# Kernel tuning notes

Hardware: AMD Instinct MI355X
Metric: run time of the kernel (lower is better)

## Reference

```python
import jax, jax.numpy as jnp
import numpy as np

B, E, D, H = 4096, 16, 512, 2048

def setup_inputs() -> dict:
    key = jax.random.key(0)
    k1, k2, k3, k4 = jax.random.split(key, 4)
    semantic_vec = jax.random.normal(k1, (B, D), dtype=jnp.float32)
    field_centers = jax.random.normal(k2, (E, D), dtype=jnp.float32)
    # Kaiming-uniform-ish Linear init scale
    lim = 1.0 / np.sqrt(D)
    W = jax.random.uniform(k3, (E, H, D), dtype=jnp.float32, minval=-lim, maxval=lim)
    b = jax.random.uniform(k4, (E, H), dtype=jnp.float32, minval=-lim, maxval=lim)
    return {"semantic_vec": semantic_vec, "field_centers": field_centers, "W": W, "b": b}

def reference(semantic_vec, field_centers, W, b):
    # Each expert e: relu((x - c_e) @ W_e^T + b_e); sum over experts.
    # Use linearity: (x - c_e) @ W_e^T = x @ W_e^T - c_e @ W_e^T, avoiding the [B,E,D] offsets tensor.
    xw = jnp.einsum('bd,ehd->beh', semantic_vec, W)          # [B,E,H]
    cw = jnp.einsum('ed,ehd->eh', field_centers, W)          # [E,H]
    pre = xw - cw[None, :, :] + b[None, :, :]                # [B,E,H]
    feature_anchor = jnp.sum(jax.nn.relu(pre), axis=1)       # [B,H]
    return feature_anchor
```

## Files before the change

kernel.cpp:

```cpp
#include <hip/hip_runtime.h>
#include <hip/hip_bf16.h>
#include <stdint.h>
#include <stddef.h>


#define B_DIM 4096
#define E_DIM 16
#define D_DIM 512
#define H_DIM 2048

typedef short bf16x8 __attribute__((ext_vector_type(8)));
typedef float f32x4 __attribute__((ext_vector_type(4)));

__device__ __forceinline__ short f2bf(float f) {
  __hip_bfloat16 h = __float2bfloat16(f);
  return *reinterpret_cast<short*>(&h);
}

__device__ __forceinline__ bf16x8 cvt8(float4 a, float4 b) {
  bf16x8 v;
  v[0] = f2bf(a.x); v[1] = f2bf(a.y); v[2] = f2bf(a.z); v[3] = f2bf(a.w);
  v[4] = f2bf(b.x); v[5] = f2bf(b.y); v[6] = f2bf(b.z); v[7] = f2bf(b.w);
  return v;
}

__device__ __forceinline__ void async_copy16(const void* gptr, void* lptr) {
  __builtin_amdgcn_global_load_lds(
      (const __attribute__((address_space(1))) void*)gptr,
      (__attribute__((address_space(3))) void*)lptr,
      16, 0, 0);
}

__global__ __launch_bounds__(256) void prep_w(
    const float* __restrict__ W, const float* __restrict__ C,
    const float* __restrict__ bias, __hip_bfloat16* __restrict__ Wb,
    float* __restrict__ bias2) {
  const int gw = (blockIdx.x * 256 + threadIdx.x) >> 6;
  const int lane = threadIdx.x & 63;
  const int e = gw >> 11;

  const float* wr = W + (size_t)gw * D_DIM + lane * 8;
  const float* cr = C + (size_t)e * D_DIM + lane * 8;
  float4 w0 = *(const float4*)(wr);
  float4 w1 = *(const float4*)(wr + 4);
  float4 c0 = *(const float4*)(cr);
  float4 c1 = *(const float4*)(cr + 4);

  *(bf16x8*)((__hip_bfloat16*)Wb + (size_t)gw * D_DIM + lane * 8) = cvt8(w0, w1);

  float dot = w0.x * c0.x + w0.y * c0.y + w0.z * c0.z + w0.w * c0.w +
              w1.x * c1.x + w1.y * c1.y + w1.z * c1.z + w1.w * c1.w;
#pragma unroll
  for (int off = 32; off > 0; off >>= 1) dot += __shfl_down(dot, off, 64);
  if (lane == 0) bias2[gw] = bias[gw] - dot;
}

__global__ __launch_bounds__(256) void conv_x(
    const float* __restrict__ X, __hip_bfloat16* __restrict__ Xb) {
  const size_t i = ((size_t)blockIdx.x * 256 + threadIdx.x) * 8;
  float4 a = *(const float4*)(X + i);
  float4 b = *(const float4*)(X + i + 4);
  *(bf16x8*)(Xb + i) = cvt8(a, b);
}

__global__ __launch_bounds__(256, 2) void moe_gemm(
    const __hip_bfloat16* __restrict__ Xb,
    const __hip_bfloat16* __restrict__ Wb,
    const float* __restrict__ bias2,
    float* __restrict__ out) {
  __shared__ __align__(16) __hip_bfloat16 As[128 * 32];
  __shared__ __align__(16) __hip_bfloat16 Bs0[128 * 32];
  __shared__ __align__(16) __hip_bfloat16 Bs1[128 * 32];
  __shared__ __align__(16) float biasS[E_DIM * 128];

  const int tid = threadIdx.x;
  const int lane = tid & 63;
  const int wave = tid >> 6;
  const int hi = blockIdx.x & 15;
  const int mi = blockIdx.x >> 4;
  const int m0 = mi * 128;
  const int h0 = hi * 128;

  for (int idx = tid; idx < E_DIM * 128; idx += 256) {
    biasS[idx] = bias2[((idx >> 7) << 11) + h0 + (idx & 127)];
  }

  const int wm = (wave & 1) * 64;
  const int wn = (wave >> 1) * 64;
  const int lm = lane & 15;
  const int q = lane >> 4;

  const int r = tid >> 2;
  const int ql = tid & 3;
  const int fr = (r ^ (r >> 2)) & 3;
  const int srcCol = ((ql ^ fr) << 3);

  const __hip_bfloat16* Asrc0 = Xb + (size_t)(m0 + r) * D_DIM + srcCol;
  const __hip_bfloat16* Asrc1 = Xb + (size_t)(m0 + r + 64) * D_DIM + srcCol;
  const size_t brow0 = (size_t)(h0 + r) * D_DIM + srcCol;
  const size_t brow1 = (size_t)(h0 + r + 64) * D_DIM + srcCol;

  int offA[4], offB[4];
#pragma unroll
  for (int i = 0; i < 4; ++i) {
    const int R = wm + i * 16 + lm;
    const int f = (R ^ (R >> 2)) & 3;
    offA[i] = R * 32 + ((q ^ f) << 3);
  }
#pragma unroll
  for (int j = 0; j < 4; ++j) {
    const int R = wn + j * 16 + lm;
    const int f = (R ^ (R >> 2)) & 3;
    offB[j] = R * 32 + ((q ^ f) << 3);
  }

  f32x4 sum[4][4];
#pragma unroll
  for (int i = 0; i < 4; ++i)
#pragma unroll
    for (int j = 0; j < 4; ++j) sum[i][j] = (f32x4){0.f, 0.f, 0.f, 0.f};

  for (int ep = 0; ep < E_DIM / 2; ++ep) {
    const __hip_bfloat16* B0 = Wb + ((size_t)(2 * ep) << 20);
    const __hip_bfloat16* B1 = Wb + ((size_t)(2 * ep + 1) << 20);

    f32x4 acc0[4][4], acc1[4][4];
#pragma unroll
    for (int i = 0; i < 4; ++i)
#pragma unroll
      for (int j = 0; j < 4; ++j) {
        acc0[i][j] = (f32x4){0.f, 0.f, 0.f, 0.f};
        acc1[i][j] = (f32x4){0.f, 0.f, 0.f, 0.f};
      }

    for (int k = 0; k < D_DIM; k += 32) {
      __syncthreads();
      async_copy16(Asrc0 + k, &As[(size_t)tid * 8]);
      async_copy16(Asrc1 + k, &As[(size_t)(tid + 256) * 8]);
      async_copy16(B0 + brow0 + k, &Bs0[(size_t)tid * 8]);
      async_copy16(B0 + brow1 + k, &Bs0[(size_t)(tid + 256) * 8]);
      async_copy16(B1 + brow0 + k, &Bs1[(size_t)tid * 8]);
      async_copy16(B1 + brow1 + k, &Bs1[(size_t)(tid + 256) * 8]);
      __syncthreads();

      bf16x8 af[4];
#pragma unroll
      for (int i = 0; i < 4; ++i) af[i] = *(const bf16x8*)&As[offA[i]];
#pragma unroll
      for (int j = 0; j < 4; ++j) {
        const bf16x8 b0 = *(const bf16x8*)&Bs0[offB[j]];
#pragma unroll
        for (int i = 0; i < 4; ++i)
          acc0[i][j] = __builtin_amdgcn_mfma_f32_16x16x32_bf16(
              af[i], b0, acc0[i][j], 0, 0, 0);
        const bf16x8 b1 = *(const bf16x8*)&Bs1[offB[j]];
#pragma unroll
        for (int i = 0; i < 4; ++i)
          acc1[i][j] = __builtin_amdgcn_mfma_f32_16x16x32_bf16(
              af[i], b1, acc1[i][j], 0, 0, 0);
      }
    }

#pragma unroll
    for (int j = 0; j < 4; ++j) {
      const float bv0 = biasS[(2 * ep) * 128 + wn + j * 16 + lm];
      const float bv1 = biasS[(2 * ep + 1) * 128 + wn + j * 16 + lm];
#pragma unroll
      for (int i = 0; i < 4; ++i)
#pragma unroll
        for (int t = 0; t < 4; ++t)
          sum[i][j][t] += fmaxf(acc0[i][j][t] + bv0, 0.f) +
                          fmaxf(acc1[i][j][t] + bv1, 0.f);
    }
  }

  const int rbase = q * 4;
#pragma unroll
  for (int i = 0; i < 4; ++i)
#pragma unroll
    for (int j = 0; j < 4; ++j)
#pragma unroll
      for (int t = 0; t < 4; ++t)
        out[(size_t)(m0 + wm + i * 16 + rbase + t) * H_DIM + h0 + wn + j * 16 + lm] =
            sum[i][j][t];
}

__global__ __launch_bounds__(256) void naive_kernel(
    const float* __restrict__ x, const float* __restrict__ c,
    const float* __restrict__ W, const float* __restrict__ bias,
    float* __restrict__ out) {
  const int idx = blockIdx.x * 256 + threadIdx.x;
  const int b = idx >> 11;
  const int h = idx & (H_DIM - 1);
  const float* xr = x + (size_t)b * D_DIM;
  float s = 0.f;
  for (int e = 0; e < E_DIM; ++e) {
    const float* wr = W + ((size_t)e * H_DIM + h) * D_DIM;
    const float* cr = c + (size_t)e * D_DIM;
    float acc = bias[e * H_DIM + h];
    for (int d = 0; d < D_DIM; ++d) acc += (xr[d] - cr[d]) * wr[d];
    s += fmaxf(acc, 0.f);
  }
  out[idx] = s;
}

extern "C" void kernel_launch(void* const* d_in, const int* in_sizes, int n_in,
                              void* d_out, int out_size, void* d_ws, size_t ws_size,
                              hipStream_t stream) {
  const float* x = (const float*)d_in[0];
  const float* c = (const float*)d_in[1];
  const float* W = (const float*)d_in[2];
  const float* b = (const float*)d_in[3];
  float* out = (float*)d_out;

  const size_t sz_wb = (size_t)E_DIM * H_DIM * D_DIM * 2;
  const size_t sz_xb = (size_t)B_DIM * D_DIM * 2;
  const size_t sz_b2 = (size_t)E_DIM * H_DIM * 4;
  const size_t need = sz_wb + sz_xb + sz_b2;

  if (ws_size >= need) {
    __hip_bfloat16* Wb = (__hip_bfloat16*)((char*)d_ws);
    __hip_bfloat16* Xb = (__hip_bfloat16*)((char*)d_ws + sz_wb);
    float* bias2 = (float*)((char*)d_ws + sz_wb + sz_xb);
    prep_w<<<8192, 256, 0, stream>>>(W, c, b, Wb, bias2);
    conv_x<<<1024, 256, 0, stream>>>(x, Xb);
    moe_gemm<<<512, 256, 0, stream>>>(Xb, Wb, bias2, out);
  } else {
    naive_kernel<<<(B_DIM * H_DIM) / 256, 256, 0, stream>>>(x, c, W, b, out);
  }
}
```

Before: 262.0 us.

## Double-buffer LDS tiles and flatten expert/k loops into one pipelined loop

Shared-memory tiles for X and the two expert weight slices are double-buffered so the async global-to-LDS copy for the next k-step is issued before computing on the current one, with a single barrier per step. The expert-pair and k loops are merged into one 128-iteration loop, with the bias+ReLU reduction applied every 16 steps. The XOR swizzle on LDS layout is removed, simplifying addressing but possibly introducing bank conflicts, and LDS usage roughly doubles, which may constrain occupancy.

```diff
diff --git a/kernel.cpp b/kernel.cpp
--- a/kernel.cpp
+++ b/kernel.cpp
@@ -68,9 +68,9 @@
     const __hip_bfloat16* __restrict__ Wb,
     const float* __restrict__ bias2,
     float* __restrict__ out) {
-  __shared__ __align__(16) __hip_bfloat16 As[128 * 32];
-  __shared__ __align__(16) __hip_bfloat16 Bs0[128 * 32];
-  __shared__ __align__(16) __hip_bfloat16 Bs1[128 * 32];
+  __shared__ __align__(16) __hip_bfloat16 As[2][128 * 32];
+  __shared__ __align__(16) __hip_bfloat16 Bs0[2][128 * 32];
+  __shared__ __align__(16) __hip_bfloat16 Bs1[2][128 * 32];
   __shared__ __align__(16) float biasS[E_DIM * 128];
 
   const int tid = threadIdx.x;
@@ -82,7 +82,7 @@
   const int h0 = hi * 128;
 
   for (int idx = tid; idx < E_DIM * 128; idx += 256) {
-    biasS[idx] = bias2[((idx >> 7) << 11) + h0 + (idx & 127)];
+    biasS[idx] = bias2[((idx >> 7) << 7 << 4) + h0 + (idx & 127)];
   }
 
   const int wm = (wave & 1) * 64;
@@ -91,88 +91,87 @@
   const int q = lane >> 4;
 
   const int r = tid >> 2;
-  const int ql = tid & 3;
-  const int fr = (r ^ (r >> 2)) & 3;
-  const int srcCol = ((ql ^ fr) << 3);
-
-  const __hip_bfloat16* Asrc0 = Xb + (size_t)(m0 + r) * D_DIM + srcCol;
-  const __hip_bfloat16* Asrc1 = Xb + (size_t)(m0 + r + 64) * D_DIM + srcCol;
-  const size_t brow0 = (size_t)(h0 + r) * D_DIM + srcCol;
-  const size_t brow1 = (size_t)(h0 + r + 64) * D_DIM + srcCol;
+  const int col = (tid & 3) << 3;
+  const size_t aOff0 = (size_t)(m0 + r) * D_DIM + col;
+  const size_t aOff1 = (size_t)(m0 + r + 64) * D_DIM + col;
+  const size_t bOff0 = (size_t)(h0 + r) * D_DIM + col;
+  const size_t bOff1 = (size_t)(h0 + r + 64) * D_DIM + col;
+  const int ld0 = tid * 8;
+  const int ld1 = (tid + 256) * 8;
 
   int offA[4], offB[4];
 #pragma unroll
-  for (int i = 0; i < 4; ++i) {
-    const int R = wm + i * 16 + lm;
-    const int f = (R ^ (R >> 2)) & 3;
-    offA[i] = R * 32 + ((q ^ f) << 3);
-  }
-#pragma unroll
-  for (int j = 0; j < 4; ++j) {
-    const int R = wn + j * 16 + lm;
-    const int f = (R ^ (R >> 2)) & 3;
-    offB[j] = R * 32 + ((q ^ f) << 3);
-  }
-
-  f32x4 sum[4][4];
+  for (int i = 0; i < 4; ++i) offA[i] = (wm + i * 16 + lm) * 32 + q * 8;
+#pragma unroll
+  for (int j = 0; j < 4; ++j) offB[j] = (wn + j * 16 + lm) * 32 + q * 8;
+
+  f32x4 sum[4][4], acc0[4][4], acc1[4][4];
 #pragma unroll
   for (int i = 0; i < 4; ++i)
 #pragma unroll
-    for (int j = 0; j < 4; ++j) sum[i][j] = (f32x4){0.f, 0.f, 0.f, 0.f};
-
-  for (int ep = 0; ep < E_DIM / 2; ++ep) {
-    const __hip_bfloat16* B0 = Wb + ((size_t)(2 * ep) << 20);
-    const __hip_bfloat16* B1 = Wb + ((size_t)(2 * ep + 1) << 20);
-
-    f32x4 acc0[4][4], acc1[4][4];
-#pragma unroll
-    for (int i = 0; i < 4; ++i)
+    for (int j = 0; j < 4; ++j) {
+      sum[i][j] = (f32x4){0.f, 0.f, 0.f, 0.f};
+      acc0[i][j] = (f32x4){0.f, 0.f, 0.f, 0.f};
+      acc1[i][j] = (f32x4){0.f, 0.f, 0.f, 0.f};
+    }
+
+#define STAGE(buf, tt)                                                       \
+  {                                                                          \
+    const int kk = ((tt) & 15) << 5;                                         \
+    const __hip_bfloat16* Bb = Wb + ((size_t)((tt) >> 4) << 21);             \
+    async_copy16(Xb + aOff0 + kk, &As[buf][ld0]);                            \
+    async_copy16(Xb + aOff1 + kk, &As[buf][ld1]);                            \
+    async_copy16(Bb + bOff0 + kk, &Bs0[buf][ld0]);                           \
+    async_copy16(Bb + bOff1 + kk, &Bs0[buf][ld1]);                           \
+    async_copy16(Bb + bOff0 + kk + (size_t)H_DIM * D_DIM, &Bs1[buf][ld0]);   \
+    async_copy16(Bb + bOff1 + kk + (size_t)H_DIM * D_DIM, &Bs1[buf][ld1]);   \
+  }
+
+  STAGE(0, 0);
+  __syncthreads();
+
+  for (int t = 0; t < 128; ++t) {
+    const int cur = t & 1;
+    if (t < 127) STAGE(cur ^ 1, t + 1);
+
+    bf16x8 af[4];
+#pragma unroll
+    for (int i = 0; i < 4; ++i) af[i] = *(const bf16x8*)&As[cur][offA[i]];
+#pragma unroll
+    for (int j = 0; j < 4; ++j) {
+      const bf16x8 b0 = *(const bf16x8*)&Bs0[cur][offB[j]];
+#pragma unroll
+      for (int i = 0; i < 4; ++i)
+        acc0[i][j] = __builtin_amdgcn_mfma_f32_16x16x32_bf16(
+            af[i], b0, acc0[i][j], 0, 0, 0);
+      const bf16x8 b1 = *(const bf16x8*)&Bs1[cur][offB[j]];
+#pragma unroll
+      for (int i = 0; i < 4; ++i)
+        acc1[i][j] = __builtin_amdgcn_mfma_f32_16x16x32_bf16(
+            af[i], b1, acc1[i][j], 0, 0, 0);
+    }
+
+    if ((t & 15) == 15) {
+      const int pair = t >> 4;
 #pragma unroll
       for (int j = 0; j < 4; ++j) {
-        acc0[i][j] = (f32x4){0.f, 0.f, 0.f, 0.f};
-        acc1[i][j] = (f32x4){0.f, 0.f, 0.f, 0.f};
-      }
-
-    for (int k = 0; k < D_DIM; k += 32) {
-      __syncthreads();
-      async_copy16(Asrc0 + k, &As[(size_t)tid * 8]);
-      async_copy16(Asrc1 + k, &As[(size_t)(tid + 256) * 8]);
-      async_copy16(B0 + brow0 + k, &Bs0[(size_t)tid * 8]);
-      async_copy16(B0 + brow1 + k, &Bs0[(size_t)(tid + 256) * 8]);
-      async_copy16(B1 + brow0 + k, &Bs1[(size_t)tid * 8]);
-      async_copy16(B1 + brow1 + k, &Bs1[(size_t)(tid + 256) * 8]);
-      __syncthreads();
-
-      bf16x8 af[4];
-#pragma unroll
-      for (int i = 0; i < 4; ++i) af[i] = *(const bf16x8*)&As[offA[i]];
-#pragma unroll
-      for (int j = 0; j < 4; ++j) {
-        const bf16x8 b0 = *(const bf16x8*)&Bs0[offB[j]];
+        const float bv0 = biasS[(2 * pair) * 128 + wn + j * 16 + lm];
+        const float bv1 = biasS[(2 * pair + 1) * 128 + wn + j * 16 + lm];
 #pragma unroll
         for (int i = 0; i < 4; ++i)
-          acc0[i][j] = __builtin_amdgcn_mfma_f32_16x16x32_bf16(
-              af[i], b0, acc0[i][j], 0, 0, 0);
-        const bf16x8 b1 = *(const bf16x8*)&Bs1[offB[j]];
-#pragma unroll
-        for (int i = 0; i < 4; ++i)
-          acc1[i][j] = __builtin_amdgcn_mfma_f32_16x16x32_bf16(
-              af[i], b1, acc1[i][j], 0, 0, 0);
+#pragma unroll
+          for (int u = 0; u < 4; ++u) {
+            sum[i][j][u] += fmaxf(acc0[i][j][u] + bv0, 0.f) +
+                            fmaxf(acc1[i][j][u] + bv1, 0.f);
+            acc0[i][j][u] = 0.f;
+            acc1[i][j][u] = 0.f;
+          }
       }
     }
 
-#pragma unroll
-    for (int j = 0; j < 4; ++j) {
-      const float bv0 = biasS[(2 * ep) * 128 + wn + j * 16 + lm];
-      const float bv1 = biasS[(2 * ep + 1) * 128 + wn + j * 16 + lm];
-#pragma unroll
-      for (int i = 0; i < 4; ++i)
-#pragma unroll
-        for (int t = 0; t < 4; ++t)
-          sum[i][j][t] += fmaxf(acc0[i][j][t] + bv0, 0.f) +
-                          fmaxf(acc1[i][j][t] + bv1, 0.f);
-    }
-  }
+    __syncthreads();
+  }
+#undef STAGE
 
   const int rbase = q * 4;
 #pragma unroll
@@ -180,9 +179,9 @@
 #pragma unroll
     for (int j = 0; j < 4; ++j)
 #pragma unroll
-      for (int t = 0; t < 4; ++t)
-        out[(size_t)(m0 + wm + i * 16 + rbase + t) * H_DIM + h0 + wn + j * 16 + lm] =
-            sum[i][j][t];
+      for (int u = 0; u < 4; ++u)
+        out[(size_t)(m0 + wm + i * 16 + rbase + u) * H_DIM + h0 + wn + j * 16 + lm] =
+            sum[i][j][u];
 }
 
 __global__ __launch_bounds__(256) void naive_kernel(
```

Result: no change. 262.3 us (+0.1%).
